# Performance work log

Hardware: AMD Instinct MI355X
Metric: run time of the kernel (lower is better)

## Reference

```python
import jax, jax.numpy as jnp
import numpy as np

D_MODEL = 768
N_HEADS = 8
D_K = 64
D_V = 64


def setup_inputs() -> dict:
    key = jax.random.key(0)
    ks = jax.random.split(key, 8)
    bs, s = 2, 2048
    q = jax.random.normal(ks[0], (bs, s, D_MODEL), dtype=jnp.float32)
    k = jax.random.normal(ks[1], (bs, s, D_MODEL), dtype=jnp.float32)
    v = jax.random.normal(ks[2], (bs, s, D_MODEL), dtype=jnp.float32)
    mask = jnp.zeros((bs, s, s), dtype=bool)
    scale = 1.0 / np.sqrt(D_MODEL)
    Wq = jax.random.normal(ks[3], (D_MODEL, N_HEADS * D_K), dtype=jnp.float32) * scale
    Wk = jax.random.normal(ks[4], (D_MODEL, N_HEADS * D_K), dtype=jnp.float32) * scale
    Wv = jax.random.normal(ks[5], (D_MODEL, N_HEADS * D_V), dtype=jnp.float32) * scale
    Wo = jax.random.normal(ks[6], (N_HEADS * D_V, D_MODEL), dtype=jnp.float32) * scale
    return {"q": q, "k": k, "v": v, "mask": mask, "Wq": Wq, "Wk": Wk, "Wv": Wv, "Wo": Wo}


def reference(q, k, v, mask, Wq, Wk, Wv, Wo):
    bs = q.shape[0]
    # projections, then split heads: (bs, n_heads, len, d_k)
    qh = (q @ Wq).reshape(bs, -1, N_HEADS, D_K).transpose(0, 2, 1, 3)
    kh = (k @ Wk).reshape(bs, -1, N_HEADS, D_K).transpose(0, 2, 1, 3)
    vh = (v @ Wv).reshape(bs, -1, N_HEADS, D_V).transpose(0, 2, 1, 3)
    # (bs, n_heads, q_len, k_len)
    scores = jnp.einsum('bhqd,bhkd->bhqk', qh, kh) / jnp.asarray(D_K ** 0.5, qh.dtype)
    scores = jnp.where(mask[:, None, :, :], jnp.asarray(-1e9, scores.dtype), scores)
    weights = jax.nn.softmax(scores, axis=-1)
    # dropout is identity at eval time
    attn = jnp.einsum('bhqk,bhkd->bhqd', weights, vh)
    attn = attn.transpose(0, 2, 1, 3).reshape(bs, -1, N_HEADS * D_V)
    output = attn @ Wo
    return (output, weights)
```

## Files before the change

### kernel.cpp

```cpp
#include <hip/hip_runtime.h>
#include <hip/hip_bf16.h>

#define DEV __device__ __forceinline__

typedef __attribute__((ext_vector_type(8))) short bf16x8;
typedef __attribute__((ext_vector_type(4))) float f32x4;

#define MFMA(a, b, c) __builtin_amdgcn_mfma_f32_16x16x32_bf16(a, b, c, 0, 0, 0)

#define BS 2
#define S 2048
#define DM 768
#define NH 8
#define DK 64
#define NPROJ 512
#define BH 16
#define KC 32
#define LOG2E 1.44269504089f

DEV unsigned short f2bf(float f) {
    unsigned int u = __float_as_uint(f);
    unsigned int r = u + 0x7fffu + ((u >> 16) & 1u);
    return (unsigned short)(r >> 16);
}

__global__ __launch_bounds__(256) void k_prep(
    const float* __restrict__ q, const float* __restrict__ k, const float* __restrict__ v,
    const unsigned char* __restrict__ mask,
    const float* __restrict__ Wq, const float* __restrict__ Wk, const float* __restrict__ Wv,
    const float* __restrict__ Wo,
    unsigned short* __restrict__ Af, unsigned long long* __restrict__ bits,
    unsigned short* __restrict__ Oq, unsigned short* __restrict__ Ok,
    unsigned short* __restrict__ Ov, unsigned short* __restrict__ Oo) {
    int blk = blockIdx.x;
    if (blk < 9216) {
        int p = blk / 3072;
        int f = (blk % 3072) * 256 + threadIdx.x;
        const float* A = (p == 0) ? q : ((p == 1) ? k : v);
        float4 x = *(const float4*)(A + (size_t)f * 4);
        int col4 = f % 192, row = f / 192;
        int c0 = col4 * 4;
        int ks = c0 >> 5, lgp = (c0 & 31) >> 3, e0 = c0 & 7;
        int rt = p * 256 + (row >> 4);
        size_t dst = ((size_t)(rt * 24 + ks) * 64 + lgp * 16 + (row & 15)) * 8 + e0;
        ushort4 o;
        o.x = f2bf(x.x); o.y = f2bf(x.y); o.z = f2bf(x.z); o.w = f2bf(x.w);
        *(ushort4*)(Af + dst) = o;
    } else if (blk < 9728) {
        int w = (blk - 9216) * 256 + threadIdx.x;
        const unsigned long long* m8 = (const unsigned long long*)(mask + (size_t)w * 64);
        unsigned long long out = 0ull;
#pragma unroll
        for (int i = 0; i < 8; i++) {
            unsigned long long xv = m8[i];
#pragma unroll
            for (int kk = 0; kk < 8; kk++)
                if ((xv >> (8 * kk)) & 0xffull) out |= 1ull << (i * 8 + kk);
        }
        bits[w] = out;
    } else {
        int i = blk - 9728;
        int ks = i % 24, byy = (i / 24) % 12, z = i / 288;
        const float* W = (z == 0) ? Wq : ((z == 1) ? Wk : ((z == 2) ? Wv : Wo));
        unsigned short* out = (z == 0) ? Oq : ((z == 1) ? Ok : ((z == 2) ? Ov : Oo));
        int N = (z == 3) ? DM : NPROJ;
        float scale = (z == 0) ? 0.125f : 1.0f;
        int wave = threadIdx.x >> 6, lane = threadIdx.x & 63;
        int nc = byy * 4 + wave;
        if (z < 3) { if (ks >= 24 || nc >= 32) return; }
        else       { if (ks >= 16) return; }
        int lr = lane & 15, lg = lane >> 4;
        int NC = N >> 4;
        const float* src = W + (size_t)(ks * 32 + lg * 8) * N + nc * 16 + lr;
        bf16x8 vv;
#pragma unroll
        for (int e = 0; e < 8; e++) vv[e] = (short)f2bf(src[(size_t)e * N] * scale);
        *(bf16x8*)(out + ((size_t)(ks * NC + nc) * 64 + lane) * 8) = vv;
    }
}

__global__ __launch_bounds__(256, 3) void k_proj(
    const unsigned short* __restrict__ Af,
    const unsigned short* __restrict__ Wfq, const unsigned short* __restrict__ Wfk,
    const unsigned short* __restrict__ Wfv,
    unsigned short* __restrict__ Qh, unsigned short* __restrict__ Kf,
    unsigned short* __restrict__ Vf) {
    __shared__ __align__(16) unsigned short ls[4096];
    int lin = blockIdx.x;
    int x = lin & 7, r = lin >> 3;
    int by = r & 3;
    int pbx = (r >> 2) * 8 + x;
    int p = pbx >> 6, bx = pbx & 63;

    const unsigned short* wf = (p == 0) ? Wfq : ((p == 1) ? Wfk : Wfv);

    const int wave = threadIdx.x >> 6, lane = threadIdx.x & 63;
    const int lr = lane & 15, lg = lane >> 4;

    f32x4 zero = {0.f, 0.f, 0.f, 0.f};
    f32x4 acc[8] = {zero, zero, zero, zero, zero, zero, zero, zero};

    const unsigned short* afb =
        Af + ((size_t)(p * 256 + bx * 4 + wave) * 24) * 512 + (size_t)lane * 8;
    bf16x8 a = *(const bf16x8*)afb;
#pragma unroll
    for (int ks = 0; ks < 24; ks++) {
        bf16x8 an;
        if (ks < 23) an = *(const bf16x8*)(afb + (ks + 1) * 512);
        const unsigned short* wp = wf + ((size_t)(ks * 32 + by * 8) * 64 + lane) * 8;
#pragma unroll
        for (int nt = 0; nt < 8; nt++) {
            bf16x8 b = *(const bf16x8*)(wp + (size_t)nt * 512);
            acc[nt] = MFMA(a, b, acc[nt]);
        }
        a = an;
    }

    const int bb = bx >> 5, kq = bx & 31;
#pragma unroll
    for (int half = 0; half < 2; half++) {
        if (half) __syncthreads();
        int h = by * 2 + half;
        int bh = bb * NH + h;
#pragma unroll
        for (int nt4 = 0; nt4 < 4; nt4++) {
            int nt = half * 4 + nt4;
#pragma unroll
            for (int j = 0; j < 4; j++) {
                unsigned short val = f2bf(acc[nt][j]);
                int lsaddr;
                if (p == 0) {
                    lsaddr = (wave * 16 + lg * 4 + j) * 64 + nt4 * 16 + lr;
                } else if (p == 1) {
                    int hh = nt4 >> 1;
                    int lgk = ((nt4 & 1) << 1) | (lr >> 3);
                    lsaddr = (wave * 2 + hh) * 512 + (lgk * 16 + lg * 4 + j) * 8 + (lr & 7);
                } else {
                    lsaddr = (nt4 * 2 + (wave >> 1)) * 512 + (lg * 16 + lr) * 8 + (wave & 1) * 4 + j;
                }
                ls[lsaddr] = val;
            }
        }
        __syncthreads();
        unsigned short* gp;
        if (p == 0)      gp = Qh + ((size_t)bh * S + kq * 64) * DK;
        else if (p == 1) gp = Kf + ((size_t)bh * KC + kq) * 4096;
        else             gp = Vf + ((size_t)bh * KC + kq) * 4096;
        const uint4* lsv = (const uint4*)ls;
        uint4 v0 = lsv[threadIdx.x * 2];
        uint4 v1 = lsv[threadIdx.x * 2 + 1];
        *(uint4*)(gp + threadIdx.x * 16) = v0;
        *(uint4*)(gp + threadIdx.x * 16 + 8) = v1;
    }
}

__global__ __launch_bounds__(256, 4) void k_lsum(
    const unsigned short* __restrict__ Qh, const unsigned short* __restrict__ Kf,
    const unsigned long long* __restrict__ mbits, float* __restrict__ lpart) {
    int lin = blockIdx.x;
    int x = lin & 7, i = lin >> 3;
    int bh = (x << 1) | (i >> 7);
    int i7 = i & 127;
    int qc = i7 >> 2, ks = i7 & 3;
    int b = bh >> 3;
    const int wave = threadIdx.x >> 6, lane = threadIdx.x & 63;
    const int lr = lane & 15, lg = lane >> 4;
    const int myrow = qc * 64 + wave * 16 + lr;

    const unsigned short* qp = Qh + ((size_t)bh * S + myrow) * DK + lg * 8;
    bf16x8 a0 = *(const bf16x8*)qp;
    bf16x8 a1 = *(const bf16x8*)(qp + 32);

    const unsigned short* kb = Kf + (size_t)bh * KC * 4096;
    const unsigned long long* mrow = mbits + (size_t)b * S * KC + (size_t)myrow * KC;

    const int kc0 = ks * 8;
    bf16x8 kf[8];
    unsigned long long wb = mrow[kc0];
#pragma unroll
    for (int u = 0; u < 8; u++)
        kf[u] = *(const bf16x8*)(kb + ((size_t)kc0 * 8 + u) * 512 + lane * 8);

    float lsum = 0.f;
    for (int kk = 0; kk < 8; kk++) {
        int kc = kc0 + kk;
        int nkc = (kk < 7) ? kc + 1 : kc;
        bf16x8 kn[8];
        unsigned long long wbn = mrow[nkc];
#pragma unroll
        for (int u = 0; u < 8; u++)
            kn[u] = *(const bf16x8*)(kb + ((size_t)nkc * 8 + u) * 512 + lane * 8);
        f32x4 s[4];
#pragma unroll
        for (int t = 0; t < 4; t++) {
            f32x4 z = {0.f, 0.f, 0.f, 0.f};
            z = MFMA(kf[t * 2], a0, z);
            z = MFMA(kf[t * 2 + 1], a1, z);
            s[t] = z;
        }
#pragma unroll
        for (int t = 0; t < 4; t++)
#pragma unroll
            for (int j = 0; j < 4; j++) {
                float p = exp2f(s[t][j] * LOG2E);
                if ((wb >> (t * 16 + lg * 4 + j)) & 1ull) p = 0.f;
                lsum += p;
            }
#pragma unroll
        for (int u = 0; u < 8; u++) kf[u] = kn[u];
        wb = wbn;
    }
    lsum += __shfl_xor(lsum, 16);
    lsum += __shfl_xor(lsum, 32);
    if (lg == 0) lpart[((size_t)bh * S + myrow) * 4 + ks] = lsum;
}

__global__ __launch_bounds__(256, 2) void k_attn(
    const unsigned short* __restrict__ Qh, const unsigned short* __restrict__ Kf,
    const unsigned short* __restrict__ Vf, const unsigned long long* __restrict__ mbits,
    const float* __restrict__ lpart, float* __restrict__ wout,
    unsigned short* __restrict__ ctxF) {
    __shared__ __align__(16) char smem[4 * 2048];
    int lin = blockIdx.x;
    int x = lin & 7, i = lin >> 3;
    int bh = (x << 1) | (i >> 5), qc = i & 31;
    int b = bh >> 3, h = bh & 7;
    const int wave = threadIdx.x >> 6, lane = threadIdx.x & 63;
    const int lr = lane & 15, lg = lane >> 4;
    const int myrow = qc * 64 + wave * 16 + lr;

    const unsigned short* qp = Qh + ((size_t)bh * S + myrow) * DK + lg * 8;
    bf16x8 a0 = *(const bf16x8*)qp;
    bf16x8 a1 = *(const bf16x8*)(qp + 32);

    const unsigned short* kb = Kf + (size_t)bh * KC * 4096;
    const unsigned short* vb = Vf + (size_t)bh * KC * 4096;
    const unsigned long long* mrow = mbits + (size_t)b * S * KC + (size_t)myrow * KC;

    f32x4 lp = *(const f32x4*)(lpart + ((size_t)bh * S + myrow) * 4);
    float ladd = -log2f(lp[0] + lp[1] + lp[2] + lp[3]);

    f32x4 zero = {0.f, 0.f, 0.f, 0.f};
    f32x4 c[4] = {zero, zero, zero, zero};
    float* wo = wout + (size_t)bh * S * S + (size_t)myrow * S;

    bf16x8 kf[8];
    unsigned long long wb = mrow[0];
#pragma unroll
    for (int u = 0; u < 8; u++)
        kf[u] = *(const bf16x8*)(kb + (size_t)u * 512 + lane * 8);

    for (int kc = 0; kc < KC; kc++) {
        int nkc = (kc + 1 < KC) ? kc + 1 : kc;
        bf16x8 kn[8], vf[8];
        unsigned long long wbn = mrow[nkc];
#pragma unroll
        for (int u = 0; u < 8; u++)
            vf[u] = *(const bf16x8*)(vb + ((size_t)kc * 8 + u) * 512 + lane * 8);
#pragma unroll
        for (int u = 0; u < 8; u++)
            kn[u] = *(const bf16x8*)(kb + ((size_t)nkc * 8 + u) * 512 + lane * 8);

        f32x4 s[4];
        __builtin_amdgcn_s_setprio(1);
#pragma unroll
        for (int t = 0; t < 4; t++) {
            f32x4 z = {0.f, 0.f, 0.f, 0.f};
            z = MFMA(kf[t * 2], a0, z);
            z = MFMA(kf[t * 2 + 1], a1, z);
            s[t] = z;
        }
        __builtin_amdgcn_s_setprio(0);

        f32x4 wv[4];
#pragma unroll
        for (int t = 0; t < 4; t++) {
#pragma unroll
            for (int j = 0; j < 4; j++) {
                float w = exp2f(__fmaf_rn(s[t][j], LOG2E, ladd));
                if ((wb >> (t * 16 + lg * 4 + j)) & 1ull) w = 0.f;
                wv[t][j] = w;
            }
            *(f32x4*)(wo + kc * 64 + t * 16 + lg * 4) = wv[t];
        }

        union { __hip_bfloat162 h2[4]; bf16x8 v8; } pa0, pa1;
        pa0.h2[0] = __float22bfloat162_rn({wv[0][0], wv[0][1]});
        pa0.h2[1] = __float22bfloat162_rn({wv[0][2], wv[0][3]});
        pa0.h2[2] = __float22bfloat162_rn({wv[1][0], wv[1][1]});
        pa0.h2[3] = __float22bfloat162_rn({wv[1][2], wv[1][3]});
        pa1.h2[0] = __float22bfloat162_rn({wv[2][0], wv[2][1]});
        pa1.h2[1] = __float22bfloat162_rn({wv[2][2], wv[2][3]});
        pa1.h2[2] = __float22bfloat162_rn({wv[3][0], wv[3][1]});
        pa1.h2[3] = __float22bfloat162_rn({wv[3][2], wv[3][3]});

        __builtin_amdgcn_s_setprio(1);
#pragma unroll
        for (int dt = 0; dt < 4; dt++) {
            c[dt] = MFMA(pa0.v8, vf[dt * 2], c[dt]);
            c[dt] = MFMA(pa1.v8, vf[dt * 2 + 1], c[dt]);
        }
        __builtin_amdgcn_s_setprio(0);

#pragma unroll
        for (int u = 0; u < 8; u++) kf[u] = kn[u];
        wb = wbn;
    }

    unsigned short* cls = (unsigned short*)(smem + wave * 2048);
#pragma unroll
    for (int dt = 0; dt < 4; dt++)
#pragma unroll
        for (int j = 0; j < 4; j++)
            cls[(dt >> 1) * 512 + (((dt & 1) * 2 + (lr >> 3)) * 16 + lg * 4 + j) * 8 + (lr & 7)] =
                f2bf(c[dt][j]);
    int rtc = b * 128 + qc * 4 + wave;
    unsigned short* gp = ctxF + ((size_t)(rtc * 16 + h * 2)) * 512 + lane * 16;
    const uint4* clsv = (const uint4*)cls;
    uint4 u0 = clsv[lane * 2];
    uint4 u1 = clsv[lane * 2 + 1];
    *(uint4*)gp = u0;
    *(uint4*)(gp + 8) = u1;
}

__global__ __launch_bounds__(256, 3) void k_outproj(const unsigned short* __restrict__ ctxF,
                                                    const unsigned short* __restrict__ wfo,
                                                    float* __restrict__ out) {
    int lin = blockIdx.x;
    int x = lin & 7, r = lin >> 3;
    int by = r >> 3, bxg = r & 7;
    int bx = bxg * 8 + x;

    const int wave = threadIdx.x >> 6, lane = threadIdx.x & 63;
    const int lr = lane & 15, lg = lane >> 4;

    f32x4 zero = {0.f, 0.f, 0.f, 0.f};
    f32x4 acc[4] = {zero, zero, zero, zero};

    const unsigned short* ap = ctxF + ((size_t)(bx * 4 + wave) * 16) * 512 + (size_t)lane * 8;
    bf16x8 a = *(const bf16x8*)ap;
#pragma unroll
    for (int ks = 0; ks < 16; ks++) {
        bf16x8 an;
        if (ks < 15) an = *(const bf16x8*)(ap + (ks + 1) * 512);
#pragma unroll
        for (int nt = 0; nt < 4; nt++) {
            const unsigned short* bp = wfo + ((size_t)(ks * 48 + by * 4 + nt) * 64 + lane) * 8;
            bf16x8 bb = *(const bf16x8*)bp;
            acc[nt] = MFMA(a, bb, acc[nt]);
        }
        a = an;
    }
#pragma unroll
    for (int nt = 0; nt < 4; nt++) {
        int col = by * 64 + nt * 16 + lr;
#pragma unroll
        for (int j = 0; j < 4; j++) {
            int rr = bx * 64 + wave * 16 + lg * 4 + j;
            out[(size_t)rr * DM + col] = acc[nt][j];
        }
    }
}

extern "C" void kernel_launch(void* const* d_in, const int* in_sizes, int n_in,
                              void* d_out, int out_size, void* d_ws, size_t ws_size,
                              hipStream_t stream) {
    const float* q = (const float*)d_in[0];
    const float* k = (const float*)d_in[1];
    const float* v = (const float*)d_in[2];
    const unsigned char* mask = (const unsigned char*)d_in[3];
    const float* Wq = (const float*)d_in[4];
    const float* Wk = (const float*)d_in[5];
    const float* Wv = (const float*)d_in[6];
    const float* Wo = (const float*)d_in[7];

    float* out = (float*)d_out;
    float* weights = out + (size_t)BS * S * DM;
    unsigned short* Af = (unsigned short*)weights;

    char* ws = (char*)d_ws;
    const size_t WT_SZ = (size_t)393216 * 2;
    const size_t HEAD_SZ = (size_t)BH * S * DK * 2;
    unsigned short* Wfq = (unsigned short*)(ws + 0 * WT_SZ);
    unsigned short* Wfk = (unsigned short*)(ws + 1 * WT_SZ);
    unsigned short* Wfv = (unsigned short*)(ws + 2 * WT_SZ);
    unsigned short* Wfo = (unsigned short*)(ws + 3 * WT_SZ);
    char* base = ws + 4 * WT_SZ;
    unsigned short* Qh = (unsigned short*)(base + 0 * HEAD_SZ);
    unsigned short* Kf = (unsigned short*)(base + 1 * HEAD_SZ);
    unsigned short* Vf = (unsigned short*)(base + 2 * HEAD_SZ);
    unsigned short* ctxF = (unsigned short*)(base + 3 * HEAD_SZ);
    unsigned long long* mbits = (unsigned long long*)(base + 4 * HEAD_SZ);
    float* lpart = (float*)(base + 4 * HEAD_SZ + 1048576);
    if (ws_size < 4 * WT_SZ + 4 * HEAD_SZ + 1048576 + (size_t)BH * S * 4 * 4) return;

    k_prep<<<10880, 256, 0, stream>>>(q, k, v, mask, Wq, Wk, Wv, Wo, Af, mbits,
                                      Wfq, Wfk, Wfv, Wfo);
    k_proj<<<768, 256, 0, stream>>>(Af, Wfq, Wfk, Wfv, Qh, Kf, Vf);
    k_lsum<<<2048, 256, 0, stream>>>(Qh, Kf, mbits, lpart);
    k_attn<<<512, 256, 0, stream>>>(Qh, Kf, Vf, mbits, lpart, weights, ctxF);
    k_outproj<<<768, 256, 0, stream>>>(ctxF, Wfo, out);
}
```

Before: 172.4 us.

## Split attention key range across two blocks and sum partial contexts in outproj

Each attention block now processes half of the key chunks, which doubles the grid to 1024 blocks and raises the occupancy hint to 4. The two partial bf16 context slices are summed inside the output projection by looping over both slices, so the split-K reduction is fused into the GEMM. The K register prefetch is dropped in favour of per-iteration loads, with a sched barrier placed before the V loads. Mask bits and lpart now live in the output buffer's scratch space to free workspace. This adds twice the context write and read traffic plus an extra rounding of the partial contexts.

```diff
diff --git a/kernel.cpp b/kernel.cpp
--- a/kernel.cpp
+++ b/kernel.cpp
@@ -17,6 +17,7 @@
 #define BH 16
 #define KC 32
 #define LOG2E 1.44269504089f
+#define CTXP_SLICE 2097152
 
 DEV unsigned short f2bf(float f) {
     unsigned int u = __float_as_uint(f);
@@ -215,15 +216,17 @@
     if (lg == 0) lpart[((size_t)bh * S + myrow) * 4 + ks] = lsum;
 }
 
-__global__ __launch_bounds__(256, 2) void k_attn(
+__global__ __launch_bounds__(256, 4) void k_attn(
     const unsigned short* __restrict__ Qh, const unsigned short* __restrict__ Kf,
     const unsigned short* __restrict__ Vf, const unsigned long long* __restrict__ mbits,
     const float* __restrict__ lpart, float* __restrict__ wout,
-    unsigned short* __restrict__ ctxF) {
+    unsigned short* __restrict__ ctxP) {
     __shared__ __align__(16) char smem[4 * 2048];
     int lin = blockIdx.x;
     int x = lin & 7, i = lin >> 3;
-    int bh = (x << 1) | (i >> 5), qc = i & 31;
+    int bh = (x << 1) | (i >> 6);
+    int rem = i & 63;
+    int qc = rem >> 1, ks2 = rem & 1;
     int b = bh >> 3, h = bh & 7;
     const int wave = threadIdx.x >> 6, lane = threadIdx.x & 63;
     const int lr = lane & 15, lg = lane >> 4;
@@ -244,22 +247,14 @@
     f32x4 c[4] = {zero, zero, zero, zero};
     float* wo = wout + (size_t)bh * S * S + (size_t)myrow * S;
 
-    bf16x8 kf[8];
-    unsigned long long wb = mrow[0];
-#pragma unroll
-    for (int u = 0; u < 8; u++)
-        kf[u] = *(const bf16x8*)(kb + (size_t)u * 512 + lane * 8);
-
-    for (int kc = 0; kc < KC; kc++) {
-        int nkc = (kc + 1 < KC) ? kc + 1 : kc;
-        bf16x8 kn[8], vf[8];
-        unsigned long long wbn = mrow[nkc];
+    const int kc0 = ks2 * 16;
+    for (int kk = 0; kk < 16; kk++) {
+        int kc = kc0 + kk;
+        unsigned long long wb = mrow[kc];
+        bf16x8 kf[8];
 #pragma unroll
         for (int u = 0; u < 8; u++)
-            vf[u] = *(const bf16x8*)(vb + ((size_t)kc * 8 + u) * 512 + lane * 8);
-#pragma unroll
-        for (int u = 0; u < 8; u++)
-            kn[u] = *(const bf16x8*)(kb + ((size_t)nkc * 8 + u) * 512 + lane * 8);
+            kf[u] = *(const bf16x8*)(kb + ((size_t)kc * 8 + u) * 512 + lane * 8);
 
         f32x4 s[4];
         __builtin_amdgcn_s_setprio(1);
@@ -271,6 +266,12 @@
             s[t] = z;
         }
         __builtin_amdgcn_s_setprio(0);
+
+        __builtin_amdgcn_sched_barrier(0);
+        bf16x8 vf[8];
+#pragma unroll
+        for (int u = 0; u < 8; u++)
+            vf[u] = *(const bf16x8*)(vb + ((size_t)kc * 8 + u) * 512 + lane * 8);
 
         f32x4 wv[4];
 #pragma unroll
@@ -301,10 +302,6 @@
             c[dt] = MFMA(pa1.v8, vf[dt * 2 + 1], c[dt]);
         }
         __builtin_amdgcn_s_setprio(0);
-
-#pragma unroll
-        for (int u = 0; u < 8; u++) kf[u] = kn[u];
-        wb = wbn;
     }
 
     unsigned short* cls = (unsigned short*)(smem + wave * 2048);
@@ -315,7 +312,8 @@
             cls[(dt >> 1) * 512 + (((dt & 1) * 2 + (lr >> 3)) * 16 + lg * 4 + j) * 8 + (lr & 7)] =
                 f2bf(c[dt][j]);
     int rtc = b * 128 + qc * 4 + wave;
-    unsigned short* gp = ctxF + ((size_t)(rtc * 16 + h * 2)) * 512 + lane * 16;
+    unsigned short* gp = ctxP + (size_t)ks2 * CTXP_SLICE +
+                         ((size_t)(rtc * 16 + h * 2)) * 512 + lane * 16;
     const uint4* clsv = (const uint4*)cls;
     uint4 u0 = clsv[lane * 2];
     uint4 u1 = clsv[lane * 2 + 1];
@@ -323,7 +321,7 @@
     *(uint4*)(gp + 8) = u1;
 }
 
-__global__ __launch_bounds__(256, 3) void k_outproj(const unsigned short* __restrict__ ctxF,
+__global__ __launch_bounds__(256, 3) void k_outproj(const unsigned short* __restrict__ ctxP,
                                                     const unsigned short* __restrict__ wfo,
                                                     float* __restrict__ out) {
     int lin = blockIdx.x;
@@ -337,19 +335,23 @@
     f32x4 zero = {0.f, 0.f, 0.f, 0.f};
     f32x4 acc[4] = {zero, zero, zero, zero};
 
-    const unsigned short* ap = ctxF + ((size_t)(bx * 4 + wave) * 16) * 512 + (size_t)lane * 8;
-    bf16x8 a = *(const bf16x8*)ap;
-#pragma unroll
-    for (int ks = 0; ks < 16; ks++) {
-        bf16x8 an;
-        if (ks < 15) an = *(const bf16x8*)(ap + (ks + 1) * 512);
-#pragma unroll
-        for (int nt = 0; nt < 4; nt++) {
-            const unsigned short* bp = wfo + ((size_t)(ks * 48 + by * 4 + nt) * 64 + lane) * 8;
-            bf16x8 bb = *(const bf16x8*)bp;
-            acc[nt] = MFMA(a, bb, acc[nt]);
-        }
-        a = an;
+#pragma unroll
+    for (int sl = 0; sl < 2; sl++) {
+        const unsigned short* ap = ctxP + (size_t)sl * CTXP_SLICE +
+                                   ((size_t)(bx * 4 + wave) * 16) * 512 + (size_t)lane * 8;
+        bf16x8 a = *(const bf16x8*)ap;
+#pragma unroll
+        for (int ks = 0; ks < 16; ks++) {
+            bf16x8 an;
+            if (ks < 15) an = *(const bf16x8*)(ap + (ks + 1) * 512);
+#pragma unroll
+            for (int nt = 0; nt < 4; nt++) {
+                const unsigned short* bp = wfo + ((size_t)(ks * 48 + by * 4 + nt) * 64 + lane) * 8;
+                bf16x8 bb = *(const bf16x8*)bp;
+                acc[nt] = MFMA(a, bb, acc[nt]);
+            }
+            a = an;
+        }
     }
 #pragma unroll
     for (int nt = 0; nt < 4; nt++) {
@@ -377,6 +379,8 @@
     float* out = (float*)d_out;
     float* weights = out + (size_t)BS * S * DM;
     unsigned short* Af = (unsigned short*)weights;
+    unsigned long long* mbits = (unsigned long long*)out;
+    float* lpart = (float*)((char*)out + 1048576);
 
     char* ws = (char*)d_ws;
     const size_t WT_SZ = (size_t)393216 * 2;
@@ -389,15 +393,13 @@
     unsigned short* Qh = (unsigned short*)(base + 0 * HEAD_SZ);
     unsigned short* Kf = (unsigned short*)(base + 1 * HEAD_SZ);
     unsigned short* Vf = (unsigned short*)(base + 2 * HEAD_SZ);
-    unsigned short* ctxF = (unsigned short*)(base + 3 * HEAD_SZ);
-    unsigned long long* mbits = (unsigned long long*)(base + 4 * HEAD_SZ);
-    float* lpart = (float*)(base + 4 * HEAD_SZ + 1048576);
-    if (ws_size < 4 * WT_SZ + 4 * HEAD_SZ + 1048576 + (size_t)BH * S * 4 * 4) return;
+    unsigned short* ctxP = (unsigned short*)(base + 3 * HEAD_SZ);
+    if (ws_size < 4 * WT_SZ + 3 * HEAD_SZ + 2 * (size_t)CTXP_SLICE * 2) return;
 
     k_prep<<<10880, 256, 0, stream>>>(q, k, v, mask, Wq, Wk, Wv, Wo, Af, mbits,
                                       Wfq, Wfk, Wfv, Wfo);
     k_proj<<<768, 256, 0, stream>>>(Af, Wfq, Wfk, Wfv, Qh, Kf, Vf);
     k_lsum<<<2048, 256, 0, stream>>>(Qh, Kf, mbits, lpart);
-    k_attn<<<512, 256, 0, stream>>>(Qh, Kf, Vf, mbits, lpart, weights, ctxF);
-    k_outproj<<<768, 256, 0, stream>>>(ctxF, Wfo, out);
-}
+    k_attn<<<1024, 256, 0, stream>>>(Qh, Kf, Vf, mbits, lpart, weights, ctxP);
+    k_outproj<<<768, 256, 0, stream>>>(ctxP, Wfo, out);
+}
```

Measured after the change: 224.2 us. 1.3x slower.
